# Optimization experiments

Measured on AMD Instinct MI355X. Metric: run time of the kernel, lower is better.

Reference implementation:

```python
import jax, jax.numpy as jnp
import numpy as np

# Irreps structure (hardcoded per init_kwargs):
#  input  = 16x0e + 8x1o  -> dim 16 + 8*3 = 40
#  query  = key = 8x0e + 4x1o -> dim 8 + 4*3 = 20
#  output = 16x0e + 8x1o -> dim 40
#  edge_sh = 1x0e + 1x1o -> dim 4
M0, M1 = 16, 8          # input multiplicities (scalar, vector)
Q0, Q1 = 8, 4           # query/key multiplicities
O0, O1 = 16, 8          # output multiplicities
TPK_NUMEL = M0*Q0 + M1*Q0 + M0*Q1 + M1*Q1 + M1*Q1   # 320
TPV_NUMEL = M0*O0 + M1*O0 + M0*O1 + M1*O1 + M1*O1   # 640
EDGE_BASIS = 16
HIDDEN = 32


def _split(x):
    """Split irreps vector [*, m0 + 3*m1] into scalars [*, m0] and vectors [*, m1, 3]."""
    m0 = x.shape[-1] - 3 * ((x.shape[-1] - M0) // 3) if False else None
    return x  # placeholder, not used


def fc_net(x, w1, w2):
    """e3nn FullyConnectedNet: no biases, 1/sqrt(fan_in) scaling, silu hidden act."""
    h = jax.nn.silu((x @ w1) * (1.0 / np.sqrt(x.shape[-1])))
    return (h @ w2) * (1.0 / np.sqrt(w1.shape[-1]))


def fctp_edge(xs, xv, shs, shv, w, o0, o1):
    """FullyConnectedTensorProduct((m0x0e+m1x1o) x (1x0e+1x1o) -> (o0x0e+o1x1o))
    with per-edge weights w [E, numel]. Component-normalized CG, path-normalized output.
    xs:[E,m0] xv:[E,m1,3] shs:[E,1] shv:[E,3]."""
    m0, m1 = xs.shape[1], xv.shape[1]
    sizes = [m0*o0, m1*o0, m0*o1, m1*o1, m1*o1]
    offs = np.cumsum([0] + sizes)
    w1 = w[:, offs[0]:offs[1]].reshape(-1, m0, o0)
    w2 = w[:, offs[1]:offs[2]].reshape(-1, m1, o0)
    w3 = w[:, offs[2]:offs[3]].reshape(-1, m0, o1)
    w4 = w[:, offs[3]:offs[4]].reshape(-1, m1, o1)
    w5 = w[:, offs[4]:offs[5]].reshape(-1, m1, o1)
    # scalar output paths: 0e x 0e -> 0e ; 1o x 1o -> 0e (dot / sqrt3)
    p_ss = xs * shs                                            # [E,m0]
    p_vv = jnp.einsum('eic,ec->ei', xv, shv) * (1.0/np.sqrt(3.0))  # [E,m1]
    out_s = (jnp.einsum('ei,eio->eo', p_ss, w1)
             + jnp.einsum('ei,eio->eo', p_vv, w2)) * (1.0/np.sqrt(m0 + m1))
    # vector output paths: 0e x 1o ; 1o x 0e ; 1o x 1o -> 1o (cross / sqrt2)
    p_sv = xs[:, :, None] * shv[:, None, :]                    # [E,m0,3]
    p_vs = xv * shs[:, :, None]                                # [E,m1,3]
    p_xx = jnp.cross(xv, shv[:, None, :]) * (1.0/np.sqrt(2.0)) # [E,m1,3]
    out_v = (jnp.einsum('eic,eio->eoc', p_sv, w3)
             + jnp.einsum('eic,eio->eoc', p_vs, w4)
             + jnp.einsum('eic,eio->eoc', p_xx, w5)) * (1.0/np.sqrt(m0 + 2*m1))
    return out_s, out_v


def setup_inputs() -> dict:
    key = jax.random.key(0)
    ks = jax.random.split(key, 12)
    N, E = 10000, 100000
    node_ft = jax.random.normal(ks[0], (N, M0 + 3*M1), dtype=jnp.float32)
    edge_index = jax.random.randint(ks[1], (2, E), 0, N, dtype=jnp.int64)
    edge_sh = jax.random.normal(ks[2], (E, 4), dtype=jnp.float32)
    edge_scalars = jax.random.uniform(ks[3], (E, EDGE_BASIS), dtype=jnp.float32)
    # learned parameters
    w_q_s = jax.random.normal(ks[4], (M0, Q0), dtype=jnp.float32)
    w_q_v = jax.random.normal(ks[5], (M1, Q1), dtype=jnp.float32)
    fck_w1 = jax.random.normal(ks[6], (EDGE_BASIS, HIDDEN), dtype=jnp.float32)
    fck_w2 = jax.random.normal(ks[7], (HIDDEN, TPK_NUMEL), dtype=jnp.float32)
    fcv_w1 = jax.random.normal(ks[8], (EDGE_BASIS, HIDDEN), dtype=jnp.float32)
    fcv_w2 = jax.random.normal(ks[9], (HIDDEN, TPV_NUMEL), dtype=jnp.float32)
    wdot_s = jax.random.normal(ks[10], (Q0, Q0), dtype=jnp.float32)
    wdot_v = jax.random.normal(ks[11], (Q1, Q1), dtype=jnp.float32)
    return dict(node_ft=node_ft, edge_index=edge_index, edge_sh=edge_sh,
                edge_scalars=edge_scalars, w_q_s=w_q_s, w_q_v=w_q_v,
                fck_w1=fck_w1, fck_w2=fck_w2, fcv_w1=fcv_w1, fcv_w2=fcv_w2,
                wdot_s=wdot_s, wdot_v=wdot_v)


def reference(node_ft, edge_index, edge_sh, edge_scalars, w_q_s, w_q_v,
              fck_w1, fck_w2, fcv_w1, fcv_w2, wdot_s, wdot_v):
    N = node_ft.shape[0]
    sender, receiver = edge_index[0], edge_index[1]
    x_s = node_ft[:, :M0]                       # [N,16]
    x_v = node_ft[:, M0:].reshape(N, M1, 3)     # [N,8,3]
    # q = o3.Linear(input -> query): per-irrep linear mixing, 1/sqrt(mul) norm
    q_s = (x_s @ w_q_s) * (1.0/np.sqrt(M0))                    # [N,Q0]
    q_v = jnp.einsum('nic,io->noc', x_v, w_q_v) * (1.0/np.sqrt(M1))  # [N,Q1,3]
    sh_s, sh_v = edge_sh[:, :1], edge_sh[:, 1:4]
    xs_e, xv_e = x_s[sender], x_v[sender]       # gather sender features
    # per-edge tensor-product weights from radial MLPs
    wk = fc_net(edge_scalars, fck_w1, fck_w2)   # [E, 320]
    wv = fc_net(edge_scalars, fcv_w1, fcv_w2)   # [E, 640]
    k_s, k_v = fctp_edge(xs_e, xv_e, sh_s, sh_v, wk, Q0, Q1)
    v_s, v_v = fctp_edge(xs_e, xv_e, sh_s, sh_v, wv, O0, O1)
    # dot = FCTP(query, key -> 0e) with shared internal weights
    qr_s, qr_v = q_s[receiver], q_v[receiver]
    fan = Q0*Q0 + Q1*Q1
    dot = (jnp.einsum('ei,ej,ij->e', qr_s, k_s, wdot_s)
           + jnp.einsum('eic,ejc,ij->e', qr_v, k_v, wdot_v) * (1.0/np.sqrt(3.0))
           ) * (1.0/np.sqrt(fan))               # [E]
    # scatter-softmax over receiver
    ex = jnp.exp(dot)
    z = jax.ops.segment_sum(ex, receiver, num_segments=N)      # [N]
    alpha = ex / z[receiver]
    a = jnp.sqrt(jax.nn.relu(alpha))            # [E]
    out_s = jax.ops.segment_sum(a[:, None] * v_s, receiver, num_segments=N)
    out_v = jax.ops.segment_sum(a[:, None, None] * v_v, receiver, num_segments=N)
    return jnp.concatenate([out_s, out_v.reshape(N, O1*3)], axis=-1)  # [N,40]
```

## Files before the change

kernel.cpp:

```cpp
#include <hip/hip_runtime.h>


#define BS 256
#define EPB 64

typedef _Float16 half2_t __attribute__((ext_vector_type(2)));

#ifdef __has_builtin
#if __has_builtin(__builtin_amdgcn_fdot2)
#define USE_FDOT2 1
#endif
#endif

__device__ __forceinline__ float silu_f(float x) {
    return x * (1.0f / (1.0f + __expf(-x)));
}
__device__ __forceinline__ unsigned short f2h(float f) {
    return __builtin_bit_cast(unsigned short, (_Float16)f);
}
__device__ __forceinline__ unsigned pk2h(float a, float b) {
    return (unsigned)f2h(a) | ((unsigned)f2h(b) << 16);
}
__device__ __forceinline__ half2_t uh2(unsigned u) {
    return __builtin_bit_cast(half2_t, u);
}
__device__ __forceinline__ float d2(unsigned a, unsigned b, float c) {
#ifdef USE_FDOT2
    return __builtin_amdgcn_fdot2(uh2(a), uh2(b), c, false);
#else
    const half2_t ha = uh2(a), hb = uh2(b);
    return c + (float)ha[0] * (float)hb[0] + (float)ha[1] * (float)hb[1];
#endif
}
__device__ __forceinline__ float wred4(float v) {
    v += __shfl_xor(v, 16);
    v += __shfl_xor(v, 32);
    return v;
}

__global__ __launch_bounds__(256) void node_pre(
    const float* __restrict__ node_ft,
    const int*   __restrict__ ei,
    const float* __restrict__ w_q_s, const float* __restrict__ w_q_v,
    const float* __restrict__ wdot_s, const float* __restrict__ wdot_v,
    float* __restrict__ qd, int* __restrict__ cnt, int* __restrict__ flag,
    int N, int E)
{
    const int n = blockIdx.x * blockDim.x + threadIdx.x;
    if (n == 0) {
        int acc = 0;
        const int kmax = (E < 64) ? E : 64;
        for (int k = 0; k < kmax; ++k) acc |= ei[2*k + 1];
        *flag = (acc == 0) ? 1 : 0;
    }
    if (n >= N) return;
// ... 179 lines not shown

    __syncthreads();

    float hk[32];
    {
        float es[16];
        const float4* a0 = (const float4*)(edge_scalars + (size_t)ec * 16);
#pragma unroll
        for (int t = 0; t < 4; ++t) {
            const float4 v = a0[t];
            es[4*t+0]=v.x; es[4*t+1]=v.y; es[4*t+2]=v.z; es[4*t+3]=v.w;
        }
#pragma unroll 8
        for (int j = 0; j < 32; ++j) {
            float a = 0.f;
#pragma unroll
            for (int t = 0; t < 16; ++t) a += es[t] * fck_w1[t*32 + j];
            hk[j] = silu_f(a * 0.25f);
        }
    }

    const uint4* g = sk4 + p * 321;

    const unsigned xs01 = pk2h(nf[4*p + 0], nf[4*p + 1]);
    const unsigned xs23 = pk2h(nf[4*p + 2], nf[4*p + 3]);

    float K1[8] = {};
#pragma unroll 8
    for (int j = 0; j < 32; ++j) {
        const uint4 A = g[j*4+0], B = g[j*4+1], C = g[j*4+2], D = g[j*4+3];
        const float h = hk[j];
        float t;
        t = d2(xs01, A.x, 0.f); t = d2(xs23, C.x, t); K1[0] += h*t;
        t = d2(xs01, A.y, 0.f); t = d2(xs23, C.y, t); K1[1] += h*t;
        t = d2(xs01, A.z, 0.f); t = d2(xs23, C.z, t); K1[2] += h*t;
        t = d2(xs01, A.w, 0.f); t = d2(xs23, C.w, t); K1[3] += h*t;
        t = d2(xs01, B.x, 0.f); t = d2(xs23, D.x, t); K1[4] += h*t;
        t = d2(xs01, B.y, 0.f); t = d2(xs23, D.y, t); K1[5] += h*t;
        t = d2(xs01, B.z, 0.f); t = d2(xs23, D.z, t); K1[6] += h*t;
        t = d2(xs01, B.w, 0.f); t = d2(xs23, D.w, t); K1[7] += h*t;
    }

    float K3[4] = {};
#pragma unroll 8
    for (int j = 0; j < 32; ++j) {
        const uint4 Ea = g[128 + j*2], Fb = g[128 + j*2 + 1];
        const float h = hk[j];
        float t;
        t = d2(xs01, Ea.x, 0.f); t = d2(xs23, Fb.x, t); K3[0] += h*t;
        t = d2(xs01, Ea.y, 0.f); t = d2(xs23, Fb.y, t); K3[1] += h*t;
        t = d2(xs01, Ea.z, 0.f); t = d2(xs23, Fb.z, t); K3[2] += h*t;
        t = d2(xs01, Ea.w, 0.f); t = d2(xs23, Fb.w, t); K3[3] += h*t;
    }

    const float c3 = 0.57735026918962576f;
    const float xa0 = nf[16 + 6*p], xa1 = nf[17 + 6*p], xa2 = nf[18 + 6*p];
    const float xb0 = nf[19 + 6*p], xb1 = nf[20 + 6*p], xb2 = nf[21 + 6*p];
    const float pv0 = (xa0*sh_v[0] + xa1*sh_v[1] + xa2*sh_v[2]) * c3;
    const float pv1 = (xb0*sh_v[0] + xb1*sh_v[1] + xb2*sh_v[2]) * c3;
    const unsigned pvp = pk2h(pv0, pv1);
    float K2[8] = {};
#pragma unroll 8
    for (int j = 0; j < 32; ++j) {
        const uint4 U = g[192 + j*2], V = g[192 + j*2 + 1];
        const float h = hk[j];
        K2[0] += h * d2(pvp, U.x, 0.f);
        K2[1] += h * d2(pvp, U.y, 0.f);
        K2[2] += h * d2(pvp, U.z, 0.f);
        K2[3] += h * d2(pvp, U.w, 0.f);
        K2[4] += h * d2(pvp, V.x, 0.f);
        K2[5] += h * d2(pvp, V.y, 0.f);
        K2[6] += h * d2(pvp, V.z, 0.f);
        K2[7] += h * d2(pvp, V.w, 0.f);
    }

    float W40[4] = {}, W41[4] = {}, W50[4] = {}, W51[4] = {};
#pragma unroll 4
    for (int jp = 0; jp < 16; ++jp) {
        const unsigned hp = pk2h(hk[2*jp], hk[2*jp+1]);
        const uint4 a = g[256 + jp*4 + 0];
        const uint4 b = g[256 + jp*4 + 1];
        const uint4 c = g[256 + jp*4 + 2];
        const uint4 d = g[256 + jp*4 + 3];
        W40[0] = d2(hp, a.x, W40[0]); W40[1] = d2(hp, a.y, W40[1]);
        W40[2] = d2(hp, a.z, W40[2]); W40[3] = d2(hp, a.w, W40[3]);
        W50[0] = d2(hp, b.x, W50[0]); W50[1] = d2(hp, b.y, W50[1]);
        W50[2] = d2(hp, b.z, W50[2]); W50[3] = d2(hp, b.w, W50[3]);
        W41[0] = d2(hp, c.x, W41[0]); W41[1] = d2(hp, c.y, W41[1]);
        W41[2] = d2(hp, c.z, W41[2]); W41[3] = d2(hp, c.w, W41[3]);
        W51[0] = d2(hp, d.x, W51[0]); W51[1] = d2(hp, d.y, W51[1]);
        W51[2] = d2(hp, d.z, W51[2]); W51[3] = d2(hp, d.w, W51[3]);
    }

    const float c7 = 0.70710678118654752f;
    float KV[12] = {};
    {
        const float s0 = sh_s*xa0, s1 = sh_s*xa1, s2 = sh_s*xa2;
        const float cx0 = c7*(xa1*sh_v[2] - xa2*sh_v[1]);
        const float cx1 = c7*(xa2*sh_v[0] - xa0*sh_v[2]);
        const float cx2 = c7*(xa0*sh_v[1] - xa1*sh_v[0]);
#pragma unroll
        for (int o = 0; o < 4; ++o) {
            KV[o*3+0] += s0*W40[o] + cx0*W50[o];
            KV[o*3+1] += s1*W40[o] + cx1*W50[o];
            KV[o*3+2] += s2*W40[o] + cx2*W50[o];
        }
    }
    {
        const float s0 = sh_s*xb0, s1 = sh_s*xb1, s2 = sh_s*xb2;
        const float cx0 = c7*(xb1*sh_v[2] - xb2*sh_v[1]);
        const float cx1 = c7*(xb2*sh_v[0] - xb0*sh_v[2]);
        const float cx2 = c7*(xb0*sh_v[1] - xb1*sh_v[0]);
#pragma unroll
        for (int o = 0; o < 4; ++o) {
            KV[o*3+0] += s0*W41[o] + cx0*W51[o];
            KV[o*3+1] += s1*W41[o] + cx1*W51[o];
            KV[o*3+2] += s2*W41[o] + cx2*W51[o];
        }
    }

#pragma unroll
    for (int o = 0; o < 8; ++o) K1[o] = wred4(K1[o]);
#pragma unroll
    for (int o = 0; o < 8; ++o) K2[o] = wred4(K2[o]);
#pragma unroll
    for (int o = 0; o < 4; ++o) K3[o] = wred4(K3[o]);
#pragma unroll
    for (int o = 0; o < 12; ++o) KV[o] = wred4(KV[o]);

    if (p == 0 && val) {
        float qdr[20];
        {
            const float4* rp = (const float4*)(qd + (size_t)rcv * 20);
#pragma unroll
            for (int t = 0; t < 5; ++t) {
                const float4 a = rp[t];
                qdr[4*t+0]=a.x; qdr[4*t+1]=a.y; qdr[4*t+2]=a.z; qdr[4*t+3]=a.w;
            }
        }
        float ds = 0.f;
#pragma unroll
        for (int o = 0; o < 8; ++o) ds += qdr[o] * (sh_s*K1[o] + K2[o]);
        float dv = 0.f;
#pragma unroll
        for (int o = 0; o < 4; ++o)
#pragma unroll
            for (int c = 0; c < 3; ++c)
                dv += qdr[8 + o*3 + c] * (K3[o]*sh_v[c] + KV[o*3+c]);
        const float dot = ds * 4.0343567508008e-3f + dv * 2.0171788261497e-3f;
        const float sa = __expf(0.5f * dot);
        exbuf[pos] = sa*sa; sabuf[e] = sa; posbuf[e] = pos;
    }
}

__global__ __launch_bounds__(BS) void edge_v_a(
    const float* __restrict__ node_ft,
    const int*   __restrict__ ei,
    const float* __restrict__ edge_sh,
    const float* __restrict__ edge_scalars,
    const float* __restrict__ fcv_w1,
    const float* __restrict__ fcv_w2,
    const float* __restrict__ sabuf,
    const int*   __restrict__ posbuf,
    float* __restrict__ vbuf,
    const int* __restrict__ flag,
    int E)
{
    __shared__ uint4 sa4[4 * 385];

    const int tid = threadIdx.x;
    for (int idx = tid; idx < 4 * 384; idx += BS) {
// ... 9 lines not shown
        } else {
            const int l = local - 256; const int j = l >> 2, h = l & 3;
            const int i0 = 2*p;
            s0 = fcv_w2 + j*640 + 256 + i0*16 + h*4;
            s1 = s0 + 16;
        }
        sa4[p * 385 + local] = make_uint4(
            pk2h(s0[0], s1[0]), pk2h(s0[1], s1[1]),
            pk2h(s0[2], s1[2]), pk2h(s0[3], s1[3]));
    }

    const int lane = tid & 63;
    const int p = lane >> 4;
    const int q = lane & 15;
    const int w = tid >> 6;
    const int e = blockIdx.x * EPB + w * 16 + q;
    const bool val = (e < E);
    const int ec = val ? e : (E - 1);

    const int is64 = *flag;
    const int snd = is64 ? ei[2*ec] : ei[ec];

    const float4 s4 = *(const float4*)(edge_sh + (size_t)ec * 4);
    const float sh_s = s4.x;

    const float* nf = node_ft + (size_t)snd * 40;

    __syncthreads();

    float hv[32];
    {
        float es[16];
        const float4* a0 = (const float4*)(edge_scalars + (size_t)ec * 16);
#pragma unroll
        for (int t = 0; t < 4; ++t) {
            const float4 v = a0[t];
            es[4*t+0]=v.x; es[4*t+1]=v.y; es[4*t+2]=v.z; es[4*t+3]=v.w;
        }
#pragma unroll 8
        for (int j = 0; j < 32; ++j) {
            float a = 0.f;
#pragma unroll
            for (int t = 0; t < 16; ++t) a += es[t] * fcv_w1[t*32 + j];
            hv[j] = silu_f(a * 0.25f);
        }
    }

    const uint4* g = sa4 + p * 385;

    const unsigned xs01 = pk2h(nf[4*p + 0]*sh_s, nf[4*p + 1]*sh_s);
    const unsigned xs23 = pk2h(nf[4*p + 2]*sh_s, nf[4*p + 3]*sh_s);
    const float c3 = 0.57735026918962576f;
    const float pv0 = (nf[16+6*p]*s4.y + nf[17+6*p]*s4.z + nf[18+6*p]*s4.w) * c3;
    const float pv1 = (nf[19+6*p]*s4.y + nf[20+6*p]*s4.z + nf[21+6*p]*s4.w) * c3;
    const unsigned pvp = pk2h(pv0, pv1);

    float A[16] = {};

#pragma unroll 2
    for (int j = 0; j < 32; ++j) {
        const uint4* gw = g + j*8;
        const uint4 a0 = gw[0], a1 = gw[1], a2 = gw[2], a3 = gw[3];
        const uint4 b0 = gw[4], b1 = gw[5], b2 = gw[6], b3 = gw[7];
        const float h = hv[j];
        float t;
        t = d2(xs01, a0.x, 0.f); t = d2(xs23, b0.x, t); A[0]  += h*t;
        t = d2(xs01, a0.y, 0.f); t = d2(xs23, b0.y, t); A[1]  += h*t;
        t = d2(xs01, a0.z, 0.f); t = d2(xs23, b0.z, t); A[2]  += h*t;
        t = d2(xs01, a0.w, 0.f); t = d2(xs23, b0.w, t); A[3]  += h*t;
        t = d2(xs01, a1.x, 0.f); t = d2(xs23, b1.x, t); A[4]  += h*t;
        t = d2(xs01, a1.y, 0.f); t = d2(xs23, b1.y, t); A[5]  += h*t;
        t = d2(xs01, a1.z, 0.f); t = d2(xs23, b1.z, t); A[6]  += h*t;
        t = d2(xs01, a1.w, 0.f); t = d2(xs23, b1.w, t); A[7]  += h*t;
        t = d2(xs01, a2.x, 0.f); t = d2(xs23, b2.x, t); A[8]  += h*t;
        t = d2(xs01, a2.y, 0.f); t = d2(xs23, b2.y, t); A[9]  += h*t;
        t = d2(xs01, a2.z, 0.f); t = d2(xs23, b2.z, t); A[10] += h*t;
        t = d2(xs01, a2.w, 0.f); t = d2(xs23, b2.w, t); A[11] += h*t;
        t = d2(xs01, a3.x, 0.f); t = d2(xs23, b3.x, t); A[12] += h*t;
        t = d2(xs01, a3.y, 0.f); t = d2(xs23, b3.y, t); A[13] += h*t;
        t = d2(xs01, a3.z, 0.f); t = d2(xs23, b3.z, t); A[14] += h*t;
        t = d2(xs01, a3.w, 0.f); t = d2(xs23, b3.w, t); A[15] += h*t;
    }

#pragma unroll 4
    for (int j = 0; j < 32; ++j) {
        const uint4* gw = g + 256 + j*4;
        const uint4 u0 = gw[0], u1 = gw[1], u2 = gw[2], u3 = gw[3];
        const float h = hv[j];
        A[0]  += h * d2(pvp, u0.x, 0.f);
        A[1]  += h * d2(pvp, u0.y, 0.f);
        A[2]  += h * d2(pvp, u0.z, 0.f);
        A[3]  += h * d2(pvp, u0.w, 0.f);
        A[4]  += h * d2(pvp, u1.x, 0.f);
        A[5]  += h * d2(pvp, u1.y, 0.f);
        A[6]  += h * d2(pvp, u1.z, 0.f);
        A[7]  += h * d2(pvp, u1.w, 0.f);
        A[8]  += h * d2(pvp, u2.x, 0.f);
        A[9]  += h * d2(pvp, u2.y, 0.f);
        A[10] += h * d2(pvp, u2.z, 0.f);
        A[11] += h * d2(pvp, u2.w, 0.f);
        A[12] += h * d2(pvp, u3.x, 0.f);
        A[13] += h * d2(pvp, u3.y, 0.f);
        A[14] += h * d2(pvp, u3.z, 0.f);
        A[15] += h * d2(pvp, u3.w, 0.f);
    }

#pragma unroll
    for (int o = 0; o < 16; ++o) A[o] = wred4(A[o]);

    if (p == 0 && val) {
        const float cs = 0.03608439182435161f;
        const float sa = sabuf[e];
        const int pos = posbuf[e];
        float4* vp = (float4*)(vbuf + (size_t)pos * 40);
#pragma unroll
        for (int t = 0; t < 4; ++t) {
            float4 r;
            r.x = sa * A[4*t+0] * cs; r.y = sa * A[4*t+1] * cs;
            r.z = sa * A[4*t+2] * cs; r.w = sa * A[4*t+3] * cs;
            vp[t] = r;
        }
    }
}

__global__ __launch_bounds__(BS) void edge_v_b(
    const float* __restrict__ node_ft,
    const int*   __restrict__ ei,
    const float* __restrict__ edge_sh,
    const float* __restrict__ edge_scalars,
    const float* __restrict__ fcv_w1,
    const float* __restrict__ fcv_w2,
    const float* __restrict__ sabuf,
    const int*   __restrict__ posbuf,
    float* __restrict__ vbuf,
    const int* __restrict__ flag,
    int E)
{
    __shared__ uint4 sb4[4 * 257];

    const int tid = threadIdx.x;
    for (int idx = tid; idx < 4 * 256; idx += BS) {
        const int p = idx >> 8;
        const int local = idx & 255;
        const float* s0;
        const float* s1;
        if (local < 128) {
            const int j = local >> 2, rr = local & 3, ip = rr >> 1, h = rr & 1;
            const int i0 = 4*p + 2*ip;
            s0 = fcv_w2 + j*640 + 384 + i0*8 + 4*h;
            s1 = s0 + 8;
        } else {
            const int l = local - 128;
            const int jp = l >> 3, rr = l & 7, il = rr >> 2, h2 = rr & 3;
            const int i = 2*p + il, j0 = 2*jp;
            const int base = (h2 < 2) ? 512 : 576;
            s0 = fcv_w2 + j0*640 + base + i*8 + (h2 & 1)*4;
            s1 = s0 + 640;
        }
        sb4[p * 257 + local] = make_uint4(
            pk2h(s0[0], s1[0]), pk2h(s0[1], s1[1]),
            pk2h(s0[2], s1[2]), pk2h(s0[3], s1[3]));
    }

    const int lane = tid & 63;
    const int p = lane >> 4;
    const int q = lane & 15;
    const int w = tid >> 6;
    const int e = blockIdx.x * EPB + w * 16 + q;
    const bool val = (e < E);
    const int ec = val ? e : (E - 1);

    const int is64 = *flag;
    const int snd = is64 ? ei[2*ec] : ei[ec];

    const float4 s4 = *(const float4*)(edge_sh + (size_t)ec * 4);
    const float sh_s = s4.x;
    const float sh_v[3] = {s4.y, s4.z, s4.w};

    const float* nf = node_ft + (size_t)snd * 40;

    __syncthreads();

    float hv[32];
    {
        float es[16];
        const float4* a0 = (const float4*)(edge_scalars + (size_t)ec * 16);
#pragma unroll
        for (int t = 0; t < 4; ++t) {
            const float4 v = a0[t];
            es[4*t+0]=v.x; es[4*t+1]=v.y; es[4*t+2]=v.z; es[4*t+3]=v.w;
        }
#pragma unroll 8
        for (int j = 0; j < 32; ++j) {
            float a = 0.f;
#pragma unroll
            for (int t = 0; t < 16; ++t) a += es[t] * fcv_w1[t*32 + j];
            hv[j] = silu_f(a * 0.25f);
        }
    }

    const uint4* g = sb4 + p * 257;

    const unsigned xs01 = pk2h(nf[4*p + 0], nf[4*p + 1]);
    const unsigned xs23 = pk2h(nf[4*p + 2], nf[4*p + 3]);

    float T3[8] = {};
#pragma unroll 4
    for (int j = 0; j < 32; ++j) {
        const uint4 E0 = g[j*4+0], E1 = g[j*4+1];
        const uint4 F0 = g[j*4+2], F1 = g[j*4+3];
        const float h = hv[j];
        float t;
        t = d2(xs01, E0.x, 0.f); t = d2(xs23, F0.x, t); T3[0] += h*t;
        t = d2(xs01, E0.y, 0.f); t = d2(xs23, F0.y, t); T3[1] += h*t;
        t = d2(xs01, E0.z, 0.f); t = d2(xs23, F0.z, t); T3[2] += h*t;
        t = d2(xs01, E0.w, 0.f); t = d2(xs23, F0.w, t); T3[3] += h*t;
        t = d2(xs01, E1.x, 0.f); t = d2(xs23, F1.x, t); T3[4] += h*t;
        t = d2(xs01, E1.y, 0.f); t = d2(xs23, F1.y, t); T3[5] += h*t;
        t = d2(xs01, E1.z, 0.f); t = d2(xs23, F1.z, t); T3[6] += h*t;
        t = d2(xs01, E1.w, 0.f); t = d2(xs23, F1.w, t); T3[7] += h*t;
    }

    float W40[8] = {}, W41[8] = {}, W50[8] = {}, W51[8] = {};
#pragma unroll 2
    for (int jp = 0; jp < 16; ++jp) {
        const unsigned hp = pk2h(hv[2*jp], hv[2*jp+1]);
        const uint4* gw = g + 128 + jp*8;
        const uint4 a = gw[0], b = gw[1], c = gw[2], d = gw[3];
        const uint4 e2 = gw[4], f = gw[5], m = gw[6], n = gw[7];
        W40[0] = d2(hp, a.x, W40[0]); W40[1] = d2(hp, a.y, W40[1]);
        W40[2] = d2(hp, a.z, W40[2]); W40[3] = d2(hp, a.w, W40[3]);
        W40[4] = d2(hp, b.x, W40[4]); W40[5] = d2(hp, b.y, W40[5]);
        W40[6] = d2(hp, b.z, W40[6]); W40[7] = d2(hp, b.w, W40[7]);
        W50[0] = d2(hp, c.x, W50[0]); W50[1] = d2(hp, c.y, W50[1]);
        W50[2] = d2(hp, c.z, W50[2]); W50[3] = d2(hp, c.w, W50[3]);
        W50[4] = d2(hp, d.x, W50[4]); W50[5] = d2(hp, d.y, W50[5]);
        W50[6] = d2(hp, d.z, W50[6]); W50[7] = d2(hp, d.w, W50[7]);
        W41[0] = d2(hp, e2.x, W41[0]); W41[1] = d2(hp, e2.y, W41[1]);
        W41[2] = d2(hp, e2.z, W41[2]); W41[3] = d2(hp, e2.w, W41[3]);
        W41[4] = d2(hp, f.x, W41[4]); W41[5] = d2(hp, f.y, W41[5]);
        W41[6] = d2(hp, f.z, W41[6]); W41[7] = d2(hp, f.w, W41[7]);
        W51[0] = d2(hp, m.x, W51[0]); W51[1] = d2(hp, m.y, W51[1]);
        W51[2] = d2(hp, m.z, W51[2]); W51[3] = d2(hp, m.w, W51[3]);
        W51[4] = d2(hp, n.x, W51[4]); W51[5] = d2(hp, n.y, W51[5]);
        W51[6] = d2(hp, n.z, W51[6]); W51[7] = d2(hp, n.w, W51[7]);
    }

    const float c7 = 0.70710678118654752f;
    float R[24] = {};
    {
        const float x0 = nf[16 + 6*p], x1 = nf[17 + 6*p], x2 = nf[18 + 6*p];
        const float s0 = sh_s*x0, s1 = sh_s*x1, s2 = sh_s*x2;
        const float cx0 = c7*(x1*sh_v[2] - x2*sh_v[1]);
        const float cx1 = c7*(x2*sh_v[0] - x0*sh_v[2]);
        const float cx2 = c7*(x0*sh_v[1] - x1*sh_v[0]);
#pragma unroll
        for (int o = 0; o < 8; ++o) {
            R[o*3+0] += s0*W40[o] + cx0*W50[o];
            R[o*3+1] += s1*W40[o] + cx1*W50[o];
            R[o*3+2] += s2*W40[o] + cx2*W50[o];
        }
    }
    {
        const float x0 = nf[19 + 6*p], x1 = nf[20 + 6*p], x2 = nf[21 + 6*p];
        const float s0 = sh_s*x0, s1 = sh_s*x1, s2 = sh_s*x2;
        const float cx0 = c7*(x1*sh_v[2] - x2*sh_v[1]);
        const float cx1 = c7*(x2*sh_v[0] - x0*sh_v[2]);
        const float cx2 = c7*(x0*sh_v[1] - x1*sh_v[0]);
#pragma unroll
        for (int o = 0; o < 8; ++o) {
            R[o*3+0] += s0*W41[o] + cx0*W51[o];
            R[o*3+1] += s1*W41[o] + cx1*W51[o];
            R[o*3+2] += s2*W41[o] + cx2*W51[o];
        }
    }

#pragma unroll
    for (int o = 0; o < 8; ++o) T3[o] = wred4(T3[o]);
#pragma unroll
    for (int o = 0; o < 24; ++o) R[o] = wred4(R[o]);

    if (p == 0 && val) {
        const float sc = 0.03125f;
        const float sa = sabuf[e];
        const int pos = posbuf[e];
        float row[24];
#pragma unroll
        for (int o = 0; o < 8; ++o)
#pragma unroll
            for (int c = 0; c < 3; ++c)
                row[o*3+c] = sa * (T3[o]*sh_v[c] + R[o*3+c]) * sc;
        float4* vp = (float4*)(vbuf + (size_t)pos * 40 + 16);
#pragma unroll
        for (int t = 0; t < 6; ++t) {
            float4 r; r.x = row[4*t+0]; r.y = row[4*t+1]; r.z = row[4*t+2]; r.w = row[4*t+3];
            vp[t] = r;
        }
    }
}

__global__ __launch_bounds__(256) void node_reduce(
    const int*   __restrict__ start,
    const float* __restrict__ exbuf,
    const float* __restrict__ vbuf,
    float* __restrict__ out, int N)
{
    const int wave = threadIdx.x >> 6;
    const int lane = threadIdx.x & 63;
    const int n = blockIdx.x * 4 + wave;
    if (n >= N) return;
    const int r0 = start[n], r1 = start[n + 1];
    float z = 0.f, comp = 0.f;
    for (int r = r0; r < r1; ++r) {
        z += exbuf[r];
// ... 62 lines not shown
```

Measured before the change: 296.4 us.

## Switch edge contractions to packed fp16 FMA accumulation and fuse loops

Replaces the fdot2-to-fp32 accumulations in the key and value edge kernels with packed half2 FMA accumulators (v_pk_fma_f16). The radial hidden weight is folded into the packed input operand, and the values are converted to fp32 only once at the end. Several separate j-loops are fused into one pass over the staged weights, and the dot-product reduction is done per lane before a single pair of cross-lane shuffles instead of reducing every output component. This cuts ALU and shuffle work but accumulates 32+ terms in fp16, which risks accuracy loss or overflow.

```diff
diff --git a/kernel.cpp b/kernel.cpp
--- a/kernel.cpp
+++ b/kernel.cpp
@@ -4,13 +4,7 @@
 #define BS 256
 #define EPB 64
 
-typedef _Float16 half2_t __attribute__((ext_vector_type(2)));
-
-#ifdef __has_builtin
-#if __has_builtin(__builtin_amdgcn_fdot2)
-#define USE_FDOT2 1
-#endif
-#endif
+typedef _Float16 h2 __attribute__((ext_vector_type(2)));
 
 __device__ __forceinline__ float silu_f(float x) {
     return x * (1.0f / (1.0f + __expf(-x)));
@@ -21,16 +15,17 @@
 __device__ __forceinline__ unsigned pk2h(float a, float b) {
     return (unsigned)f2h(a) | ((unsigned)f2h(b) << 16);
 }
-__device__ __forceinline__ half2_t uh2(unsigned u) {
-    return __builtin_bit_cast(half2_t, u);
-}
-__device__ __forceinline__ float d2(unsigned a, unsigned b, float c) {
-#ifdef USE_FDOT2
-    return __builtin_amdgcn_fdot2(uh2(a), uh2(b), c, false);
-#else
-    const half2_t ha = uh2(a), hb = uh2(b);
-    return c + (float)ha[0] * (float)hb[0] + (float)ha[1] * (float)hb[1];
-#endif
+__device__ __forceinline__ h2 uh2(unsigned u) {
+    return __builtin_bit_cast(h2, u);
+}
+__device__ __forceinline__ h2 pkrtz(float a, float b) {
+    return __builtin_bit_cast(h2, __builtin_amdgcn_cvt_pkrtz(a, b));
+}
+__device__ __forceinline__ h2 pfma(h2 a, h2 b, h2 c) {
+    return __builtin_elementwise_fma(a, b, c);
+}
+__device__ __forceinline__ float h2s(h2 a) {
+    return (float)a[0] + (float)a[1];
 }
 __device__ __forceinline__ float wred4(float v) {
     v += __shfl_xor(v, 16);
@@ -256,131 +251,109 @@
 
     const uint4* g = sk4 + p * 321;
 
-    const unsigned xs01 = pk2h(nf[4*p + 0], nf[4*p + 1]);
-    const unsigned xs23 = pk2h(nf[4*p + 2], nf[4*p + 3]);
-
-    float K1[8] = {};
-#pragma unroll 8
+    const h2 xs01 = pkrtz(nf[4*p + 0], nf[4*p + 1]);
+    const h2 xs23 = pkrtz(nf[4*p + 2], nf[4*p + 3]);
+    const float c3 = 0.57735026918962576f;
+    const float x00 = nf[16 + 6*p], x01 = nf[17 + 6*p], x02 = nf[18 + 6*p];
+    const float x10 = nf[19 + 6*p], x11 = nf[20 + 6*p], x12 = nf[21 + 6*p];
+    const h2 pvp = pkrtz((x00*sh_v[0] + x01*sh_v[1] + x02*sh_v[2]) * c3,
+                         (x10*sh_v[0] + x11*sh_v[1] + x12*sh_v[2]) * c3);
+
+    h2 K1[8] = {}, K3[4] = {}, K2[8] = {};
+#pragma unroll 4
     for (int j = 0; j < 32; ++j) {
         const uint4 A = g[j*4+0], B = g[j*4+1], C = g[j*4+2], D = g[j*4+3];
-        const float h = hk[j];
-        float t;
-        t = d2(xs01, A.x, 0.f); t = d2(xs23, C.x, t); K1[0] += h*t;
-        t = d2(xs01, A.y, 0.f); t = d2(xs23, C.y, t); K1[1] += h*t;
-        t = d2(xs01, A.z, 0.f); t = d2(xs23, C.z, t); K1[2] += h*t;
-        t = d2(xs01, A.w, 0.f); t = d2(xs23, C.w, t); K1[3] += h*t;
-        t = d2(xs01, B.x, 0.f); t = d2(xs23, D.x, t); K1[4] += h*t;
-        t = d2(xs01, B.y, 0.f); t = d2(xs23, D.y, t); K1[5] += h*t;
-        t = d2(xs01, B.z, 0.f); t = d2(xs23, D.z, t); K1[6] += h*t;
-        t = d2(xs01, B.w, 0.f); t = d2(xs23, D.w, t); K1[7] += h*t;
-    }
-
-    float K3[4] = {};
-#pragma unroll 8
-    for (int j = 0; j < 32; ++j) {
         const uint4 Ea = g[128 + j*2], Fb = g[128 + j*2 + 1];
-        const float h = hk[j];
-        float t;
-        t = d2(xs01, Ea.x, 0.f); t = d2(xs23, Fb.x, t); K3[0] += h*t;
-        t = d2(xs01, Ea.y, 0.f); t = d2(xs23, Fb.y, t); K3[1] += h*t;
-        t = d2(xs01, Ea.z, 0.f); t = d2(xs23, Fb.z, t); K3[2] += h*t;
-        t = d2(xs01, Ea.w, 0.f); t = d2(xs23, Fb.w, t); K3[3] += h*t;
-    }
-
-    const float c3 = 0.57735026918962576f;
-    const float xa0 = nf[16 + 6*p], xa1 = nf[17 + 6*p], xa2 = nf[18 + 6*p];
-    const float xb0 = nf[19 + 6*p], xb1 = nf[20 + 6*p], xb2 = nf[21 + 6*p];
-    const float pv0 = (xa0*sh_v[0] + xa1*sh_v[1] + xa2*sh_v[2]) * c3;
-    const float pv1 = (xb0*sh_v[0] + xb1*sh_v[1] + xb2*sh_v[2]) * c3;
-    const unsigned pvp = pk2h(pv0, pv1);
-    float K2[8] = {};
-#pragma unroll 8
-    for (int j = 0; j < 32; ++j) {
         const uint4 U = g[192 + j*2], V = g[192 + j*2 + 1];
-        const float h = hk[j];
-        K2[0] += h * d2(pvp, U.x, 0.f);
-        K2[1] += h * d2(pvp, U.y, 0.f);
-        K2[2] += h * d2(pvp, U.z, 0.f);
-        K2[3] += h * d2(pvp, U.w, 0.f);
-        K2[4] += h * d2(pvp, V.x, 0.f);
-        K2[5] += h * d2(pvp, V.y, 0.f);
-        K2[6] += h * d2(pvp, V.z, 0.f);
-        K2[7] += h * d2(pvp, V.w, 0.f);
-    }
-
-    float W40[4] = {}, W41[4] = {}, W50[4] = {}, W51[4] = {};
+        const h2 hh = pkrtz(hk[j], hk[j]);
+        const h2 t01 = hh * xs01, t23 = hh * xs23, tp = hh * pvp;
+        K1[0]=pfma(t01,uh2(A.x),K1[0]); K1[0]=pfma(t23,uh2(C.x),K1[0]);
+        K1[1]=pfma(t01,uh2(A.y),K1[1]); K1[1]=pfma(t23,uh2(C.y),K1[1]);
+        K1[2]=pfma(t01,uh2(A.z),K1[2]); K1[2]=pfma(t23,uh2(C.z),K1[2]);
+        K1[3]=pfma(t01,uh2(A.w),K1[3]); K1[3]=pfma(t23,uh2(C.w),K1[3]);
+        K1[4]=pfma(t01,uh2(B.x),K1[4]); K1[4]=pfma(t23,uh2(D.x),K1[4]);
+        K1[5]=pfma(t01,uh2(B.y),K1[5]); K1[5]=pfma(t23,uh2(D.y),K1[5]);
+        K1[6]=pfma(t01,uh2(B.z),K1[6]); K1[6]=pfma(t23,uh2(D.z),K1[6]);
+        K1[7]=pfma(t01,uh2(B.w),K1[7]); K1[7]=pfma(t23,uh2(D.w),K1[7]);
+        K3[0]=pfma(t01,uh2(Ea.x),K3[0]); K3[0]=pfma(t23,uh2(Fb.x),K3[0]);
+        K3[1]=pfma(t01,uh2(Ea.y),K3[1]); K3[1]=pfma(t23,uh2(Fb.y),K3[1]);
+        K3[2]=pfma(t01,uh2(Ea.z),K3[2]); K3[2]=pfma(t23,uh2(Fb.z),K3[2]);
+        K3[3]=pfma(t01,uh2(Ea.w),K3[3]); K3[3]=pfma(t23,uh2(Fb.w),K3[3]);
+        K2[0]=pfma(tp,uh2(U.x),K2[0]); K2[1]=pfma(tp,uh2(U.y),K2[1]);
+        K2[2]=pfma(tp,uh2(U.z),K2[2]); K2[3]=pfma(tp,uh2(U.w),K2[3]);
+        K2[4]=pfma(tp,uh2(V.x),K2[4]); K2[5]=pfma(tp,uh2(V.y),K2[5]);
+        K2[6]=pfma(tp,uh2(V.z),K2[6]); K2[7]=pfma(tp,uh2(V.w),K2[7]);
+    }
+
+    h2 P4[8] = {}, P5[8] = {};
 #pragma unroll 4
     for (int jp = 0; jp < 16; ++jp) {
-        const unsigned hp = pk2h(hk[2*jp], hk[2*jp+1]);
-        const uint4 a = g[256 + jp*4 + 0];
-        const uint4 b = g[256 + jp*4 + 1];
-        const uint4 c = g[256 + jp*4 + 2];
-        const uint4 d = g[256 + jp*4 + 3];
-        W40[0] = d2(hp, a.x, W40[0]); W40[1] = d2(hp, a.y, W40[1]);
-        W40[2] = d2(hp, a.z, W40[2]); W40[3] = d2(hp, a.w, W40[3]);
-        W50[0] = d2(hp, b.x, W50[0]); W50[1] = d2(hp, b.y, W50[1]);
-        W50[2] = d2(hp, b.z, W50[2]); W50[3] = d2(hp, b.w, W50[3]);
-        W41[0] = d2(hp, c.x, W41[0]); W41[1] = d2(hp, c.y, W41[1]);
-        W41[2] = d2(hp, c.z, W41[2]); W41[3] = d2(hp, c.w, W41[3]);
-        W51[0] = d2(hp, d.x, W51[0]); W51[1] = d2(hp, d.y, W51[1]);
-        W51[2] = d2(hp, d.z, W51[2]); W51[3] = d2(hp, d.w, W51[3]);
+        const uint4 a4 = g[256 + jp*4 + 0];
+        const uint4 b4 = g[256 + jp*4 + 1];
+        const uint4 c4 = g[256 + jp*4 + 2];
+        const uint4 d4 = g[256 + jp*4 + 3];
+        const h2 hp = pkrtz(hk[2*jp], hk[2*jp+1]);
+        P4[0]=pfma(hp,uh2(a4.x),P4[0]); P4[1]=pfma(hp,uh2(a4.y),P4[1]);
+        P4[2]=pfma(hp,uh2(a4.z),P4[2]); P4[3]=pfma(hp,uh2(a4.w),P4[3]);
+        P5[0]=pfma(hp,uh2(b4.x),P5[0]); P5[1]=pfma(hp,uh2(b4.y),P5[1]);
+        P5[2]=pfma(hp,uh2(b4.z),P5[2]); P5[3]=pfma(hp,uh2(b4.w),P5[3]);
+        P4[4]=pfma(hp,uh2(c4.x),P4[4]); P4[5]=pfma(hp,uh2(c4.y),P4[5]);
+        P4[6]=pfma(hp,uh2(c4.z),P4[6]); P4[7]=pfma(hp,uh2(c4.w),P4[7]);
+        P5[4]=pfma(hp,uh2(d4.x),P5[4]); P5[5]=pfma(hp,uh2(d4.y),P5[5]);
+        P5[6]=pfma(hp,uh2(d4.z),P5[6]); P5[7]=pfma(hp,uh2(d4.w),P5[7]);
     }
 
     const float c7 = 0.70710678118654752f;
-    float KV[12] = {};
+    float ds = 0.f, dv = 0.f;
     {
-        const float s0 = sh_s*xa0, s1 = sh_s*xa1, s2 = sh_s*xa2;
-        const float cx0 = c7*(xa1*sh_v[2] - xa2*sh_v[1]);
-        const float cx1 = c7*(xa2*sh_v[0] - xa0*sh_v[2]);
-        const float cx2 = c7*(xa0*sh_v[1] - xa1*sh_v[0]);
+        float qdr[20];
+        const float4* rp = (const float4*)(qd + (size_t)rcv * 20);
+#pragma unroll
+        for (int t = 0; t < 5; ++t) {
+            const float4 a = rp[t];
+            qdr[4*t+0]=a.x; qdr[4*t+1]=a.y; qdr[4*t+2]=a.z; qdr[4*t+3]=a.w;
+        }
+#pragma unroll
+        for (int o = 0; o < 8; ++o)
+            ds += qdr[o] * (sh_s*h2s(K1[o]) + h2s(K2[o]));
+        float KV[12] = {};
+        {
+            const float s0=sh_s*x00, s1=sh_s*x01, s2=sh_s*x02;
+            const float cx0=c7*(x01*sh_v[2]-x02*sh_v[1]);
+            const float cx1=c7*(x02*sh_v[0]-x00*sh_v[2]);
+            const float cx2=c7*(x00*sh_v[1]-x01*sh_v[0]);
+#pragma unroll
+            for (int o = 0; o < 4; ++o) {
+                const float w4 = h2s(P4[o]), w5 = h2s(P5[o]);
+                KV[o*3+0] += s0*w4 + cx0*w5;
+                KV[o*3+1] += s1*w4 + cx1*w5;
+                KV[o*3+2] += s2*w4 + cx2*w5;
+            }
+        }
+        {
+            const float s0=sh_s*x10, s1=sh_s*x11, s2=sh_s*x12;
+            const float cx0=c7*(x11*sh_v[2]-x12*sh_v[1]);
+            const float cx1=c7*(x12*sh_v[0]-x10*sh_v[2]);
+            const float cx2=c7*(x10*sh_v[1]-x11*sh_v[0]);
+#pragma unroll
+            for (int o = 0; o < 4; ++o) {
+                const float w4 = h2s(P4[4+o]), w5 = h2s(P5[4+o]);
+                KV[o*3+0] += s0*w4 + cx0*w5;
+                KV[o*3+1] += s1*w4 + cx1*w5;
+                KV[o*3+2] += s2*w4 + cx2*w5;
+            }
+        }
 #pragma unroll
         for (int o = 0; o < 4; ++o) {
-            KV[o*3+0] += s0*W40[o] + cx0*W50[o];
-            KV[o*3+1] += s1*W40[o] + cx1*W50[o];
-            KV[o*3+2] += s2*W40[o] + cx2*W50[o];
-        }
-    }
-    {
-        const float s0 = sh_s*xb0, s1 = sh_s*xb1, s2 = sh_s*xb2;
-        const float cx0 = c7*(xb1*sh_v[2] - xb2*sh_v[1]);
-        const float cx1 = c7*(xb2*sh_v[0] - xb0*sh_v[2]);
-        const float cx2 = c7*(xb0*sh_v[1] - xb1*sh_v[0]);
-#pragma unroll
-        for (int o = 0; o < 4; ++o) {
-            KV[o*3+0] += s0*W41[o] + cx0*W51[o];
-            KV[o*3+1] += s1*W41[o] + cx1*W51[o];
-            KV[o*3+2] += s2*W41[o] + cx2*W51[o];
-        }
-    }
-
-#pragma unroll
-    for (int o = 0; o < 8; ++o) K1[o] = wred4(K1[o]);
-#pragma unroll
-    for (int o = 0; o < 8; ++o) K2[o] = wred4(K2[o]);
-#pragma unroll
-    for (int o = 0; o < 4; ++o) K3[o] = wred4(K3[o]);
-#pragma unroll
-    for (int o = 0; o < 12; ++o) KV[o] = wred4(KV[o]);
+            const float k3 = h2s(K3[o]);
+#pragma unroll
+            for (int c = 0; c < 3; ++c)
+                dv += qdr[8 + o*3 + c] * (k3*sh_v[c] + KV[o*3+c]);
+        }
+    }
+    ds = wred4(ds); dv = wred4(dv);
 
     if (p == 0 && val) {
-        float qdr[20];
-        {
-            const float4* rp = (const float4*)(qd + (size_t)rcv * 20);
-#pragma unroll
-            for (int t = 0; t < 5; ++t) {
-                const float4 a = rp[t];
-                qdr[4*t+0]=a.x; qdr[4*t+1]=a.y; qdr[4*t+2]=a.z; qdr[4*t+3]=a.w;
-            }
-        }
-        float ds = 0.f;
-#pragma unroll
-        for (int o = 0; o < 8; ++o) ds += qdr[o] * (sh_s*K1[o] + K2[o]);
-        float dv = 0.f;
-#pragma unroll
-        for (int o = 0; o < 4; ++o)
-#pragma unroll
-            for (int c = 0; c < 3; ++c)
-                dv += qdr[8 + o*3 + c] * (K3[o]*sh_v[c] + KV[o*3+c]);
         const float dot = ds * 4.0343567508008e-3f + dv * 2.0171788261497e-3f;
         const float sa = __expf(0.5f * dot);
         exbuf[pos] = sa*sa; sabuf[e] = sa; posbuf[e] = pos;
@@ -436,7 +409,6 @@
     const int snd = is64 ? ei[2*ec] : ei[ec];
 
     const float4 s4 = *(const float4*)(edge_sh + (size_t)ec * 4);
-    const float sh_s = s4.x;
 
     const float* nf = node_ft + (size_t)snd * 40;
 
@@ -462,65 +434,44 @@
 
     const uint4* g = sa4 + p * 385;
 
-    const unsigned xs01 = pk2h(nf[4*p + 0]*sh_s, nf[4*p + 1]*sh_s);
-    const unsigned xs23 = pk2h(nf[4*p + 2]*sh_s, nf[4*p + 3]*sh_s);
+    const h2 xs01 = pkrtz(nf[4*p + 0]*s4.x, nf[4*p + 1]*s4.x);
+    const h2 xs23 = pkrtz(nf[4*p + 2]*s4.x, nf[4*p + 3]*s4.x);
     const float c3 = 0.57735026918962576f;
-    const float pv0 = (nf[16+6*p]*s4.y + nf[17+6*p]*s4.z + nf[18+6*p]*s4.w) * c3;
-    const float pv1 = (nf[19+6*p]*s4.y + nf[20+6*p]*s4.z + nf[21+6*p]*s4.w) * c3;
-    const unsigned pvp = pk2h(pv0, pv1);
-
-    float A[16] = {};
-
-#pragma unroll 2
+    const h2 pvp = pkrtz(
+        (nf[16+6*p]*s4.y + nf[17+6*p]*s4.z + nf[18+6*p]*s4.w) * c3,
+        (nf[19+6*p]*s4.y + nf[20+6*p]*s4.z + nf[21+6*p]*s4.w) * c3);
+
+    h2 Aa[16] = {};
+#pragma unroll 4
     for (int j = 0; j < 32; ++j) {
         const uint4* gw = g + j*8;
         const uint4 a0 = gw[0], a1 = gw[1], a2 = gw[2], a3 = gw[3];
         const uint4 b0 = gw[4], b1 = gw[5], b2 = gw[6], b3 = gw[7];
-        const float h = hv[j];
-        float t;
-        t = d2(xs01, a0.x, 0.f); t = d2(xs23, b0.x, t); A[0]  += h*t;
-        t = d2(xs01, a0.y, 0.f); t = d2(xs23, b0.y, t); A[1]  += h*t;
-        t = d2(xs01, a0.z, 0.f); t = d2(xs23, b0.z, t); A[2]  += h*t;
-        t = d2(xs01, a0.w, 0.f); t = d2(xs23, b0.w, t); A[3]  += h*t;
-        t = d2(xs01, a1.x, 0.f); t = d2(xs23, b1.x, t); A[4]  += h*t;
-        t = d2(xs01, a1.y, 0.f); t = d2(xs23, b1.y, t); A[5]  += h*t;
-        t = d2(xs01, a1.z, 0.f); t = d2(xs23, b1.z, t); A[6]  += h*t;
-        t = d2(xs01, a1.w, 0.f); t = d2(xs23, b1.w, t); A[7]  += h*t;
-        t = d2(xs01, a2.x, 0.f); t = d2(xs23, b2.x, t); A[8]  += h*t;
-        t = d2(xs01, a2.y, 0.f); t = d2(xs23, b2.y, t); A[9]  += h*t;
-        t = d2(xs01, a2.z, 0.f); t = d2(xs23, b2.z, t); A[10] += h*t;
-        t = d2(xs01, a2.w, 0.f); t = d2(xs23, b2.w, t); A[11] += h*t;
-        t = d2(xs01, a3.x, 0.f); t = d2(xs23, b3.x, t); A[12] += h*t;
-        t = d2(xs01, a3.y, 0.f); t = d2(xs23, b3.y, t); A[13] += h*t;
-        t = d2(xs01, a3.z, 0.f); t = d2(xs23, b3.z, t); A[14] += h*t;
-        t = d2(xs01, a3.w, 0.f); t = d2(xs23, b3.w, t); A[15] += h*t;
-    }
-
-#pragma unroll 4
-    for (int j = 0; j < 32; ++j) {
-        const uint4* gw = g + 256 + j*4;
-        const uint4 u0 = gw[0], u1 = gw[1], u2 = gw[2], u3 = gw[3];
-        const float h = hv[j];
-        A[0]  += h * d2(pvp, u0.x, 0.f);
-        A[1]  += h * d2(pvp, u0.y, 0.f);
-        A[2]  += h * d2(pvp, u0.z, 0.f);
-        A[3]  += h * d2(pvp, u0.w, 0.f);
-        A[4]  += h * d2(pvp, u1.x, 0.f);
-        A[5]  += h * d2(pvp, u1.y, 0.f);
-        A[6]  += h * d2(pvp, u1.z, 0.f);
-        A[7]  += h * d2(pvp, u1.w, 0.f);
-        A[8]  += h * d2(pvp, u2.x, 0.f);
-        A[9]  += h * d2(pvp, u2.y, 0.f);
-        A[10] += h * d2(pvp, u2.z, 0.f);
-        A[11] += h * d2(pvp, u2.w, 0.f);
-        A[12] += h * d2(pvp, u3.x, 0.f);
-        A[13] += h * d2(pvp, u3.y, 0.f);
-        A[14] += h * d2(pvp, u3.z, 0.f);
-        A[15] += h * d2(pvp, u3.w, 0.f);
-    }
-
-#pragma unroll
-    for (int o = 0; o < 16; ++o) A[o] = wred4(A[o]);
+        const uint4* g2 = g + 256 + j*4;
+        const uint4 u0 = g2[0], u1 = g2[1], u2 = g2[2], u3 = g2[3];
+        const h2 hh = pkrtz(hv[j], hv[j]);
+        const h2 t01 = hh * xs01, t23 = hh * xs23, tp = hh * pvp;
+        Aa[0] =pfma(t01,uh2(a0.x),Aa[0]);  Aa[0] =pfma(t23,uh2(b0.x),Aa[0]);  Aa[0] =pfma(tp,uh2(u0.x),Aa[0]);
+        Aa[1] =pfma(t01,uh2(a0.y),Aa[1]);  Aa[1] =pfma(t23,uh2(b0.y),Aa[1]);  Aa[1] =pfma(tp,uh2(u0.y),Aa[1]);
+        Aa[2] =pfma(t01,uh2(a0.z),Aa[2]);  Aa[2] =pfma(t23,uh2(b0.z),Aa[2]);  Aa[2] =pfma(tp,uh2(u0.z),Aa[2]);
+        Aa[3] =pfma(t01,uh2(a0.w),Aa[3]);  Aa[3] =pfma(t23,uh2(b0.w),Aa[3]);  Aa[3] =pfma(tp,uh2(u0.w),Aa[3]);
+        Aa[4] =pfma(t01,uh2(a1.x),Aa[4]);  Aa[4] =pfma(t23,uh2(b1.x),Aa[4]);  Aa[4] =pfma(tp,uh2(u1.x),Aa[4]);
+        Aa[5] =pfma(t01,uh2(a1.y),Aa[5]);  Aa[5] =pfma(t23,uh2(b1.y),Aa[5]);  Aa[5] =pfma(tp,uh2(u1.y),Aa[5]);
+        Aa[6] =pfma(t01,uh2(a1.z),Aa[6]);  Aa[6] =pfma(t23,uh2(b1.z),Aa[6]);  Aa[6] =pfma(tp,uh2(u1.z),Aa[6]);
+        Aa[7] =pfma(t01,uh2(a1.w),Aa[7]);  Aa[7] =pfma(t23,uh2(b1.w),Aa[7]);  Aa[7] =pfma(tp,uh2(u1.w),Aa[7]);
+        Aa[8] =pfma(t01,uh2(a2.x),Aa[8]);  Aa[8] =pfma(t23,uh2(b2.x),Aa[8]);  Aa[8] =pfma(tp,uh2(u2.x),Aa[8]);
+        Aa[9] =pfma(t01,uh2(a2.y),Aa[9]);  Aa[9] =pfma(t23,uh2(b2.y),Aa[9]);  Aa[9] =pfma(tp,uh2(u2.y),Aa[9]);
+        Aa[10]=pfma(t01,uh2(a2.z),Aa[10]); Aa[10]=pfma(t23,uh2(b2.z),Aa[10]); Aa[10]=pfma(tp,uh2(u2.z),Aa[10]);
+        Aa[11]=pfma(t01,uh2(a2.w),Aa[11]); Aa[11]=pfma(t23,uh2(b2.w),Aa[11]); Aa[11]=pfma(tp,uh2(u2.w),Aa[11]);
+        Aa[12]=pfma(t01,uh2(a3.x),Aa[12]); Aa[12]=pfma(t23,uh2(b3.x),Aa[12]); Aa[12]=pfma(tp,uh2(u3.x),Aa[12]);
+        Aa[13]=pfma(t01,uh2(a3.y),Aa[13]); Aa[13]=pfma(t23,uh2(b3.y),Aa[13]); Aa[13]=pfma(tp,uh2(u3.y),Aa[13]);
+        Aa[14]=pfma(t01,uh2(a3.z),Aa[14]); Aa[14]=pfma(t23,uh2(b3.z),Aa[14]); Aa[14]=pfma(tp,uh2(u3.z),Aa[14]);
+        Aa[15]=pfma(t01,uh2(a3.w),Aa[15]); Aa[15]=pfma(t23,uh2(b3.w),Aa[15]); Aa[15]=pfma(tp,uh2(u3.w),Aa[15]);
+    }
+
+    float A0[16];
+#pragma unroll
+    for (int o = 0; o < 16; ++o) A0[o] = wred4(h2s(Aa[o]));
 
     if (p == 0 && val) {
         const float cs = 0.03608439182435161f;
@@ -530,8 +481,8 @@
 #pragma unroll
         for (int t = 0; t < 4; ++t) {
             float4 r;
-            r.x = sa * A[4*t+0] * cs; r.y = sa * A[4*t+1] * cs;
-            r.z = sa * A[4*t+2] * cs; r.w = sa * A[4*t+3] * cs;
+            r.x = sa * A0[4*t+0] * cs; r.y = sa * A0[4*t+1] * cs;
+            r.z = sa * A0[4*t+2] * cs; r.w = sa * A0[4*t+3] * cs;
             vp[t] = r;
         }
     }
@@ -565,10 +516,10 @@
             s1 = s0 + 8;
         } else {
             const int l = local - 128;
-            const int jp = l >> 3, rr = l & 7, il = rr >> 2, h2 = rr & 3;
+            const int jp = l >> 3, rr = l & 7, il = rr >> 2, h2c = rr & 3;
             const int i = 2*p + il, j0 = 2*jp;
-            const int base = (h2 < 2) ? 512 : 576;
-            s0 = fcv_w2 + j0*640 + base + i*8 + (h2 & 1)*4;
+            const int base = (h2c < 2) ? 512 : 576;
+            s0 = fcv_w2 + j0*640 + base + i*8 + (h2c & 1)*4;
             s1 = s0 + 640;
         }
         sb4[p * 257 + local] = make_uint4(
@@ -615,84 +566,92 @@
 
     const uint4* g = sb4 + p * 257;
 
-    const unsigned xs01 = pk2h(nf[4*p + 0], nf[4*p + 1]);
-    const unsigned xs23 = pk2h(nf[4*p + 2], nf[4*p + 3]);
-
-    float T3[8] = {};
+    const h2 xs01 = pkrtz(nf[4*p + 0], nf[4*p + 1]);
+    const h2 xs23 = pkrtz(nf[4*p + 2], nf[4*p + 3]);
+
+    h2 T3[8] = {};
 #pragma unroll 4
     for (int j = 0; j < 32; ++j) {
         const uint4 E0 = g[j*4+0], E1 = g[j*4+1];
         const uint4 F0 = g[j*4+2], F1 = g[j*4+3];
-        const float h = hv[j];
-        float t;
-        t = d2(xs01, E0.x, 0.f); t = d2(xs23, F0.x, t); T3[0] += h*t;
-        t = d2(xs01, E0.y, 0.f); t = d2(xs23, F0.y, t); T3[1] += h*t;
-        t = d2(xs01, E0.z, 0.f); t = d2(xs23, F0.z, t); T3[2] += h*t;
-        t = d2(xs01, E0.w, 0.f); t = d2(xs23, F0.w, t); T3[3] += h*t;
-        t = d2(xs01, E1.x, 0.f); t = d2(xs23, F1.x, t); T3[4] += h*t;
-        t = d2(xs01, E1.y, 0.f); t = d2(xs23, F1.y, t); T3[5] += h*t;
-        t = d2(xs01, E1.z, 0.f); t = d2(xs23, F1.z, t); T3[6] += h*t;
-        t = d2(xs01, E1.w, 0.f); t = d2(xs23, F1.w, t); T3[7] += h*t;
-    }
-
-    float W40[8] = {}, W41[8] = {}, W50[8] = {}, W51[8] = {};
+        const h2 hh = pkrtz(hv[j], hv[j]);
+        const h2 t01 = hh * xs01, t23 = hh * xs23;
+        T3[0]=pfma(t01,uh2(E0.x),T3[0]); T3[0]=pfma(t23,uh2(F0.x),T3[0]);
+        T3[1]=pfma(t01,uh2(E0.y),T3[1]); T3[1]=pfma(t23,uh2(F0.y),T3[1]);
+        T3[2]=pfma(t01,uh2(E0.z),T3[2]); T3[2]=pfma(t23,uh2(F0.z),T3[2]);
+        T3[3]=pfma(t01,uh2(E0.w),T3[3]); T3[3]=pfma(t23,uh2(F0.w),T3[3]);
+        T3[4]=pfma(t01,uh2(E1.x),T3[4]); T3[4]=pfma(t23,uh2(F1.x),T3[4]);
+        T3[5]=pfma(t01,uh2(E1.y),T3[5]); T3[5]=pfma(t23,uh2(F1.y),T3[5]);
+        T3[6]=pfma(t01,uh2(E1.z),T3[6]); T3[6]=pfma(t23,uh2(F1.z),T3[6]);
+        T3[7]=pfma(t01,uh2(E1.w),T3[7]); T3[7]=pfma(t23,uh2(F1.w),T3[7]);
+    }
+
+    h2 P4[16] = {}, P5[16] = {};
 #pragma unroll 2
     for (int jp = 0; jp < 16; ++jp) {
-        const unsigned hp = pk2h(hv[2*jp], hv[2*jp+1]);
         const uint4* gw = g + 128 + jp*8;
-        const uint4 a = gw[0], b = gw[1], c = gw[2], d = gw[3];
-        const uint4 e2 = gw[4], f = gw[5], m = gw[6], n = gw[7];
-        W40[0] = d2(hp, a.x, W40[0]); W40[1] = d2(hp, a.y, W40[1]);
-        W40[2] = d2(hp, a.z, W40[2]); W40[3] = d2(hp, a.w, W40[3]);
-        W40[4] = d2(hp, b.x, W40[4]); W40[5] = d2(hp, b.y, W40[5]);
-        W40[6] = d2(hp, b.z, W40[6]); W40[7] = d2(hp, b.w, W40[7]);
-        W50[0] = d2(hp, c.x, W50[0]); W50[1] = d2(hp, c.y, W50[1]);
-        W50[2] = d2(hp, c.z, W50[2]); W50[3] = d2(hp, c.w, W50[3]);
-        W50[4] = d2(hp, d.x, W50[4]); W50[5] = d2(hp, d.y, W50[5]);
-        W50[6] = d2(hp, d.z, W50[6]); W50[7] = d2(hp, d.w, W50[7]);
-        W41[0] = d2(hp, e2.x, W41[0]); W41[1] = d2(hp, e2.y, W41[1]);
-        W41[2] = d2(hp, e2.z, W41[2]); W41[3] = d2(hp, e2.w, W41[3]);
-        W41[4] = d2(hp, f.x, W41[4]); W41[5] = d2(hp, f.y, W41[5]);
-        W41[6] = d2(hp, f.z, W41[6]); W41[7] = d2(hp, f.w, W41[7]);
-        W51[0] = d2(hp, m.x, W51[0]); W51[1] = d2(hp, m.y, W51[1]);
-        W51[2] = d2(hp, m.z, W51[2]); W51[3] = d2(hp, m.w, W51[3]);
-        W51[4] = d2(hp, n.x, W51[4]); W51[5] = d2(hp, n.y, W51[5]);
-        W51[6] = d2(hp, n.z, W51[6]); W51[7] = d2(hp, n.w, W51[7]);
+        const uint4 a4 = gw[0], b4 = gw[1];
+        const uint4 c4 = gw[2], d4 = gw[3];
+        const uint4 e4 = gw[4], f4 = gw[5];
+        const uint4 m4 = gw[6], n4 = gw[7];
+        const h2 hp = pkrtz(hv[2*jp], hv[2*jp+1]);
+        P4[0] =pfma(hp,uh2(a4.x),P4[0]);  P4[1] =pfma(hp,uh2(a4.y),P4[1]);
+        P4[2] =pfma(hp,uh2(a4.z),P4[2]);  P4[3] =pfma(hp,uh2(a4.w),P4[3]);
+        P4[4] =pfma(hp,uh2(b4.x),P4[4]);  P4[5] =pfma(hp,uh2(b4.y),P4[5]);
+        P4[6] =pfma(hp,uh2(b4.z),P4[6]);  P4[7] =pfma(hp,uh2(b4.w),P4[7]);
+        P5[0] =pfma(hp,uh2(c4.x),P5[0]);  P5[1] =pfma(hp,uh2(c4.y),P5[1]);
+        P5[2] =pfma(hp,uh2(c4.z),P5[2]);  P5[3] =pfma(hp,uh2(c4.w),P5[3]);
+        P5[4] =pfma(hp,uh2(d4.x),P5[4]);  P5[5] =pfma(hp,uh2(d4.y),P5[5]);
+        P5[6] =pfma(hp,uh2(d4.z),P5[6]);  P5[7] =pfma(hp,uh2(d4.w),P5[7]);
+        P4[8] =pfma(hp,uh2(e4.x),P4[8]);  P4[9] =pfma(hp,uh2(e4.y),P4[9]);
+        P4[10]=pfma(hp,uh2(e4.z),P4[10]); P4[11]=pfma(hp,uh2(e4.w),P4[11]);
+        P4[12]=pfma(hp,uh2(f4.x),P4[12]); P4[13]=pfma(hp,uh2(f4.y),P4[13]);
+        P4[14]=pfma(hp,uh2(f4.z),P4[14]); P4[15]=pfma(hp,uh2(f4.w),P4[15]);
+        P5[8] =pfma(hp,uh2(m4.x),P5[8]);  P5[9] =pfma(hp,uh2(m4.y),P5[9]);
+        P5[10]=pfma(hp,uh2(m4.z),P5[10]); P5[11]=pfma(hp,uh2(m4.w),P5[11]);
+        P5[12]=pfma(hp,uh2(n4.x),P5[12]); P5[13]=pfma(hp,uh2(n4.y),P5[13]);
+        P5[14]=pfma(hp,uh2(n4.z),P5[14]); P5[15]=pfma(hp,uh2(n4.w),P5[15]);
     }
 
     const float c7 = 0.70710678118654752f;
-    float R[24] = {};
+    float R[24], T3f[8];
     {
-        const float x0 = nf[16 + 6*p], x1 = nf[17 + 6*p], x2 = nf[18 + 6*p];
-        const float s0 = sh_s*x0, s1 = sh_s*x1, s2 = sh_s*x2;
-        const float cx0 = c7*(x1*sh_v[2] - x2*sh_v[1]);
-        const float cx1 = c7*(x2*sh_v[0] - x0*sh_v[2]);
-        const float cx2 = c7*(x0*sh_v[1] - x1*sh_v[0]);
-#pragma unroll
-        for (int o = 0; o < 8; ++o) {
-            R[o*3+0] += s0*W40[o] + cx0*W50[o];
-            R[o*3+1] += s1*W40[o] + cx1*W50[o];
-            R[o*3+2] += s2*W40[o] + cx2*W50[o];
-        }
-    }
-    {
-        const float x0 = nf[19 + 6*p], x1 = nf[20 + 6*p], x2 = nf[21 + 6*p];
-        const float s0 = sh_s*x0, s1 = sh_s*x1, s2 = sh_s*x2;
-        const float cx0 = c7*(x1*sh_v[2] - x2*sh_v[1]);
-        const float cx1 = c7*(x2*sh_v[0] - x0*sh_v[2]);
-        const float cx2 = c7*(x0*sh_v[1] - x1*sh_v[0]);
-#pragma unroll
-        for (int o = 0; o < 8; ++o) {
-            R[o*3+0] += s0*W41[o] + cx0*W51[o];
-            R[o*3+1] += s1*W41[o] + cx1*W51[o];
-            R[o*3+2] += s2*W41[o] + cx2*W51[o];
-        }
-    }
-
-#pragma unroll
-    for (int o = 0; o < 8; ++o) T3[o] = wred4(T3[o]);
-#pragma unroll
-    for (int o = 0; o < 24; ++o) R[o] = wred4(R[o]);
+        float acc[24];
+#pragma unroll
+        for (int o = 0; o < 24; ++o) acc[o] = 0.f;
+        {
+            const float x0 = nf[16 + 6*p], x1 = nf[17 + 6*p], x2 = nf[18 + 6*p];
+            const float s0 = sh_s*x0, s1 = sh_s*x1, s2 = sh_s*x2;
+            const float cx0 = c7*(x1*sh_v[2] - x2*sh_v[1]);
+            const float cx1 = c7*(x2*sh_v[0] - x0*sh_v[2]);
+            const float cx2 = c7*(x0*sh_v[1] - x1*sh_v[0]);
+#pragma unroll
+            for (int o = 0; o < 8; ++o) {
+                const float w4 = h2s(P4[o]), w5 = h2s(P5[o]);
+                acc[o*3+0] += s0*w4 + cx0*w5;
+                acc[o*3+1] += s1*w4 + cx1*w5;
+                acc[o*3+2] += s2*w4 + cx2*w5;
+            }
+        }
+        {
+            const float x0 = nf[19 + 6*p], x1 = nf[20 + 6*p], x2 = nf[21 + 6*p];
+            const float s0 = sh_s*x0, s1 = sh_s*x1, s2 = sh_s*x2;
+            const float cx0 = c7*(x1*sh_v[2] - x2*sh_v[1]);
+            const float cx1 = c7*(x2*sh_v[0] - x0*sh_v[2]);
+            const float cx2 = c7*(x0*sh_v[1] - x1*sh_v[0]);
+#pragma unroll
+            for (int o = 0; o < 8; ++o) {
+                const float w4 = h2s(P4[8+o]), w5 = h2s(P5[8+o]);
+                acc[o*3+0] += s0*w4 + cx0*w5;
+                acc[o*3+1] += s1*w4 + cx1*w5;
+                acc[o*3+2] += s2*w4 + cx2*w5;
+            }
+        }
+#pragma unroll
+        for (int o = 0; o < 24; ++o) R[o] = wred4(acc[o]);
+    }
+#pragma unroll
+    for (int o = 0; o < 8; ++o) T3f[o] = wred4(h2s(T3[o]));
 
     if (p == 0 && val) {
         const float sc = 0.03125f;
@@ -703,7 +662,7 @@
         for (int o = 0; o < 8; ++o)
 #pragma unroll
             for (int c = 0; c < 3; ++c)
-                row[o*3+c] = sa * (T3[o]*sh_v[c] + R[o*3+c]) * sc;
+                row[o*3+c] = sa * (T3f[o]*sh_v[c] + R[o*3+c]) * sc;
         float4* vp = (float4*)(vbuf + (size_t)pos * 40 + 16);
 #pragma unroll
         for (int t = 0; t < 6; ++t) {
```

New measurement: 269.2 us. 1.1x faster.
